# Kernel tuning notes

Hardware: AMD Instinct MI355X
Metric: run time of the kernel (lower is better)

## Reference

```python
import jax, jax.numpy as jnp
import numpy as np

B, T, I, H, D = 4, 4096, 1024, 16, 64


def setup_inputs() -> dict:
    key = jax.random.key(0)
    k1, k2, k3 = jax.random.split(key, 3)
    inputs = jax.random.normal(k1, (B, T, I), dtype=jnp.float32)
    kv_kernel = jax.random.normal(k2, (I, H, D, 2), dtype=jnp.float32) * (1.0 / np.sqrt(I))
    q_kernel = jax.random.normal(k3, (H, D), dtype=jnp.float32) * (1.0 / np.sqrt(D))
    return {"inputs": inputs, "kv_kernel": kv_kernel, "q_kernel": q_kernel}


def _combine(a, b):
    # state layout along last axis: [m (1), u (1), w (D)]
    ma, ua, wa = a[..., :1], a[..., 1:2], a[..., 2:]
    mb, ub, wb = b[..., :1], b[..., 1:2], b[..., 2:]
    m = jnp.maximum(ma, mb)
    ea = jnp.exp(ma - m)
    eb = jnp.exp(mb - m)
    return jnp.concatenate([m, ua * ea + ub * eb, wa * ea + wb * eb], axis=-1)


def reference(inputs, kv_kernel, q_kernel):
    # inputs: (B,T,I); kv_kernel: (I,H,D,2); q_kernel: (H,D)
    kv = jnp.einsum('bti,ihdk->bthdk', inputs, kv_kernel)
    kv = jax.nn.silu(kv)
    k = kv[..., 0]  # (B,T,H,D)
    v = kv[..., 1]  # (B,T,H,D)
    st = jnp.einsum('hd,bthd->bth', q_kernel, k)[..., None]  # (B,T,H,1)
    u_init = jnp.ones_like(st)
    elems = jnp.concatenate([st, u_init, v], axis=-1)  # (B,T,H,2+D)
    o = jax.lax.associative_scan(_combine, elems, axis=1)
    c = o[..., 1:2]  # denominator (B,T,H,1)
    a = o[..., 2:]   # numerator   (B,T,H,D)
    h = a / c        # (B,T,H,D)
    # concat_heads=False -> mean over heads
    return jnp.mean(h, axis=-2)  # (B,T,D)
```

## Files before the change

kernel.cpp:

```cpp
#include <hip/hip_runtime.h>
#include <hip/hip_bf16.h>
#include <math.h>

constexpr int B_ = 4, T_ = 4096, I_ = 1024, H_ = 16, D_ = 64;
constexpr int M_ = B_ * T_;
constexpr int N_ = H_ * D_ * 2;
constexpr int C_ = 64;
constexpr int L_ = T_ / C_;
constexpr int NT_ = 16;

typedef __bf16 bf16x8 __attribute__((ext_vector_type(8)));
typedef float  f32x4  __attribute__((ext_vector_type(4)));

__device__ __forceinline__ float silu_f(float x) {
    return x / (1.0f + __expf(-x));
}

__device__ __forceinline__ ushort f2bf_u(float x) {
    unsigned u = __float_as_uint(x);
    unsigned r = (u + 0x7fffu + ((u >> 16) & 1u)) >> 16;
    return (ushort)r;
}
__device__ __forceinline__ float bfu2f(ushort u) {
    return __uint_as_float(((unsigned)u) << 16);
}

__device__ __forceinline__ void gload_lds16(const void* g, void* l) {
    __builtin_amdgcn_global_load_lds(
        (const __attribute__((address_space(1))) unsigned int*)g,
        (__attribute__((address_space(3))) unsigned int*)l, 16, 0, 0);
}

__global__ __launch_bounds__(256) void convert_a_kernel(
    const float* __restrict__ A, ushort* __restrict__ A2)
{
    int idx = blockIdx.x * 256 + threadIdx.x;
    int m  = idx >> 8;
    int kq = (idx & 255) * 4;
    float4 a = *reinterpret_cast<const float4*>(&A[(size_t)m * 1024 + kq]);
    ushort4 hi;
    hi.x = f2bf_u(a.x);
    hi.y = f2bf_u(a.y);
    hi.z = f2bf_u(a.z);
    hi.w = f2bf_u(a.w);
    *reinterpret_cast<ushort4*>(&A2[(size_t)m * 1024 + kq]) = hi;
}

__global__ __launch_bounds__(256) void convert_bT_kernel(
    const float* __restrict__ Bm, ushort* __restrict__ B2T)
{
    __shared__ float tile[64][65];
    const int k0 = blockIdx.x * 64;
    const int n0 = blockIdx.y * 64;
    const int tid = threadIdx.x;
    #pragma unroll
    for (int p = 0; p < 4; ++p) {
        int f = tid + p * 256;
        int r  = f >> 4;
        int c4 = (f & 15) * 4;
        float4 v = *reinterpret_cast<const float4*>(
            &Bm[(size_t)(k0 + r) * 2048 + n0 + c4]);
        tile[r][c4 + 0] = v.x; tile[r][c4 + 1] = v.y;
        tile[r][c4 + 2] = v.z; tile[r][c4 + 3] = v.w;
    }
    __syncthreads();
    #pragma unroll
    for (int p = 0; p < 4; ++p) {
        int f = tid + p * 256;
        int n  = f >> 4;
        int kq = (f & 15) * 4;
        ushort4 hi;
        hi.x = f2bf_u(tile[kq + 0][n]);
        hi.y = f2bf_u(tile[kq + 1][n]);
        hi.z = f2bf_u(tile[kq + 2][n]);
        hi.w = f2bf_u(tile[kq + 3][n]);
        *reinterpret_cast<ushort4*>(&B2T[(size_t)(n0 + n) * 1024 + k0 + kq]) = hi;
    }
}

__device__ __forceinline__ int akof(int t) { return t * 64; }
__device__ __forceinline__ int bkof(int t) { return t * 64; }

#define BARRIER do { asm volatile("" ::: "memory"); \
    __builtin_amdgcn_s_barrier(); \
    asm volatile("" ::: "memory"); } while (0)
#define WAITLGKM asm volatile("s_waitcnt lgkmcnt(0)" ::: "memory")
#define WAITVM(n) asm volatile("s_waitcnt vmcnt(" #n ")" ::: "memory")

#define STAGE(gptr, kb, ldsoff, rs2) do { \
    gload_lds16((gptr) + (kb),         lds + (ldsoff) + tid * 8); \
    gload_lds16((gptr) + (kb) + (rs2), lds + (ldsoff) + 4096 + tid * 8); \
} while (0)

#define RDA(ab, i, kk) (*reinterpret_cast<const bf16x8*>((ab) + (i) * 1024 + ((kk) ? ck1 : ck0)))
#define RDB(bb, j, kk) (*reinterpret_cast<const bf16x8*>((bb) + (j) * 1024 + ((kk) ? ck1 : ck0)))

#define PH_READ_A(ab, ibase) do { \
    _Pragma("unroll") for (int i_ = 0; i_ < 4; ++i_) { \
        a[i_][0] = RDA(ab, (ibase) + i_, 0); \
        a[i_][1] = RDA(ab, (ibase) + i_, 1); } } while (0)
#define PH_READ_B(bb, breg, jbase) do { \
    _Pragma("unroll") for (int j_ = 0; j_ < 2; ++j_) { \
        breg[j_][0] = RDB(bb, (jbase) + j_, 0); \
        breg[j_][1] = RDB(bb, (jbase) + j_, 1); } } while (0)

#define QUAD(IH, BREG, JB) do { \
    __builtin_amdgcn_s_setprio(1); \
    _Pragma("unroll") for (int i_ = 0; i_ < 4; ++i_) \
    _Pragma("unroll") for (int j_ = 0; j_ < 2; ++j_) \
    _Pragma("unroll") for (int k_ = 0; k_ < 2; ++k_) \
        acc[(IH) + i_][(JB) + j_] = __builtin_amdgcn_mfma_f32_16x16x32_bf16( \
            a[i_][k_], BREG[j_][k_], acc[(IH) + i_][(JB) + j_], 0, 0, 0); \
    __builtin_amdgcn_s_setprio(0); \
} while (0)

__global__ __launch_bounds__(512, 2) void gemm_mfma8_kernel(
    const ushort* __restrict__ A2,
    const ushort* __restrict__ B2T,
    const float* __restrict__ qk,
    ushort* __restrict__ v_buf,
    float* __restrict__ s_buf)
{
    __shared__ ushort lds[65536];
    __shared__ float spart[8][128];

    const int bid = blockIdx.x;
    const int swz = (bid & 7) * 64 + (bid >> 3);
    const int bx  = swz >> 6;
    const int by  = swz & 63;
    const int m0  = by * 256;
    const int n0  = bx * 256;

    const int tid  = threadIdx.x;
    const int lane = tid & 63;
    const int wid  = tid >> 6;
    const int wr = wid >> 2, wc = wid & 3;
    const int l15 = lane & 15, lg = lane >> 4;

    const int row0 = tid >> 3;
    const int ch0  = (tid & 7) ^ (row0 & 7);
    const ushort* pA  = A2  + (size_t)(m0 + row0) * 1024 + ch0 * 8;
    const ushort* pB  = B2T + (size_t)(n0 + row0) * 1024 + ch0 * 8;
    const ushort* pA1 = pA + 128 * 1024;
    const ushort* pB1 = pB + 128 * 1024;

    const int ck0 = ((0 + lg) ^ (l15 & 7)) * 8;
    const int ck1 = ((4 + lg) ^ (l15 & 7)) * 8;
    const ushort* aB0 = lds + (wr * 128 + l15) * 64;
    const ushort* bB0 = lds + 16384 + (wc * 64 + l15) * 64;
    const ushort* aB1 = aB0 + 32768;
    const ushort* bB1 = bB0 + 32768;

    f32x4 acc[8][4];
    #pragma unroll
    for (int i = 0; i < 8; ++i)
        #pragma unroll
        for (int j = 0; j < 4; ++j)
            acc[i][j] = (f32x4){0.f, 0.f, 0.f, 0.f};
    bf16x8 a[4][2], b01[2][2], b23[2][2];

    {
        const int ak0 = akof(0), bk0 = bkof(0);
        const int ak1 = akof(1), bk1 = bkof(1);
        STAGE(pA,  ak0, 0,             65536);
        STAGE(pA1, ak0, 8192,          65536);
        STAGE(pB,  bk0, 16384,         65536);
        STAGE(pB1, bk0, 16384 + 8192,  65536);
        STAGE(pB,  bk1, 49152,         65536);
        STAGE(pA,  ak1, 32768,         65536);
        WAITVM(4);
        BARRIER;
    }

    for (int I = 0; I < NT_ / 2 - 1; ++I) {
        const int t1g = 2 * I + 1, t2g = 2 * I + 2, t3g = 2 * I + 3;
        const int ak1 = akof(t1g), bk1 = bkof(t1g);
        const int ak2 = akof(t2g), bk2 = bkof(t2g);
        const int ak3 = akof(t3g), bk3 = bkof(t3g);
        PH_READ_A(aB0, 0); PH_READ_B(bB0, b01, 0);
        STAGE(pA1, ak1, 32768 + 8192, 65536);
        BARRIER; WAITLGKM; QUAD(0, b01, 0); BARRIER;
        PH_READ_B(bB0, b23, 2);
        STAGE(pB1, bk1, 49152 + 8192, 65536);
        BARRIER; WAITLGKM; QUAD(0, b23, 2); BARRIER;
        PH_READ_A(aB0, 4);
        STAGE(pB, bk2, 16384, 65536);
        BARRIER; WAITLGKM; QUAD(4, b01, 0); BARRIER;
        STAGE(pA, ak2, 0, 65536);
        WAITVM(4);
        BARRIER; QUAD(4, b23, 2); BARRIER;
        PH_READ_A(aB1, 0); PH_READ_B(bB1, b01, 0);
        STAGE(pA1, ak2, 8192, 65536);
        BARRIER; WAITLGKM; QUAD(0, b01, 0); BARRIER;
        PH_READ_B(bB1, b23, 2);
        STAGE(pB1, bk2, 16384 + 8192, 65536);
        BARRIER; WAITLGKM; QUAD(0, b23, 2); BARRIER;
        PH_READ_A(aB1, 4);
        STAGE(pB, bk3, 49152, 65536);
        BARRIER; WAITLGKM; QUAD(4, b01, 0); BARRIER;
        STAGE(pA, ak3, 32768, 65536);
        WAITVM(4);
        BARRIER; QUAD(4, b23, 2); BARRIER;
    }

    {
        const int t1g = NT_ - 1;
        const int ak1 = akof(t1g), bk1 = bkof(t1g);
        PH_READ_A(aB0, 0); PH_READ_B(bB0, b01, 0);
        STAGE(pA1, ak1, 32768 + 8192, 65536);
        BARRIER; WAITLGKM; QUAD(0, b01, 0); BARRIER;
        PH_READ_B(bB0, b23, 2);
        STAGE(pB1, bk1, 49152 + 8192, 65536);
        BARRIER; WAITLGKM; QUAD(0, b23, 2); BARRIER;
        PH_READ_A(aB0, 4);
        BARRIER; WAITLGKM; QUAD(4, b01, 0); BARRIER;
        WAITVM(0);
        BARRIER; QUAD(4, b23, 2); BARRIER;
        PH_READ_A(aB1, 0); PH_READ_B(bB1, b01, 0);
        BARRIER; WAITLGKM; QUAD(0, b01, 0); BARRIER;
        PH_READ_B(bB1, b23, 2);
        BARRIER; WAITLGKM; QUAD(0, b23, 2); BARRIER;
        PH_READ_A(aB1, 4);
        BARRIER; WAITLGKM; QUAD(4, b01, 0); BARRIER;
        QUAD(4, b23, 2);
    }

    const int hloc  = wc >> 1;
    const int h     = 2 * bx + hloc;
    const int dbase = (wc & 1) * 32 + (l15 >> 1);
    float qv[4];
    #pragma unroll
    for (int j = 0; j < 4; ++j) qv[j] = qk[h * 64 + dbase + j * 8];
    const bool kcol = ((l15 & 1) == 0);

    #pragma unroll
    for (int i = 0; i < 8; ++i) {
        #pragma unroll
        for (int rr = 0; rr < 4; ++rr) {
            int m = m0 + wr * 128 + i * 16 + lg * 4 + rr;
            int b = m >> 12, tt = m & 4095;
            float p = 0.f;
            #pragma unroll
            for (int j = 0; j < 4; ++j) {
                float sv = silu_f(acc[i][j][rr]);
                if (kcol) {
                    p += qv[j] * sv;
                } else {
                    v_buf[((size_t)(b * H_ + h) * T_ + tt) * D_ + dbase + j * 8] =
                        f2bf_u(sv);
                }
            }
            p += __shfl_xor(p, 2);
            p += __shfl_xor(p, 4);
            p += __shfl_xor(p, 8);
            if (l15 == 0) spart[wid][i * 16 + lg * 4 + rr] = p;
        }
    }
    __syncthreads();
    {
        int wr2 = tid >> 8, hl = (tid >> 7) & 1, row = tid & 127;
        int m = m0 + wr2 * 128 + row;
        int b = m >> 12, tt = m & 4095;
        s_buf[(size_t)(b * H_ + 2 * bx + hl) * T_ + tt] =
            spart[wr2 * 4 + hl * 2][row] + spart[wr2 * 4 + hl * 2 + 1][row];
    }
}

#define TILE_M 128
#define TILE_N 128
#define TILE_K 16
__global__ __launch_bounds__(256) void gemm_kv_kernel(
    const float* __restrict__ A, const float* __restrict__ Bm,
    const float* __restrict__ q, ushort* __restrict__ v_buf,
    float* __restrict__ s_buf)
{
    __shared__ float As[TILE_K][TILE_M + 4];
    __shared__ float Bs[TILE_K][TILE_N + 4];
    const int tid = threadIdx.x;
    const int h   = blockIdx.x;
    const int bm  = blockIdx.y;
    const int m0  = bm * TILE_M;
    const int n0  = h * TILE_N;
    const int tx = tid & 15, ty = tid >> 4;
    float acc[8][8];
    #pragma unroll
    for (int i = 0; i < 8; ++i)
        #pragma unroll
        for (int j = 0; j < 8; ++j) acc[i][j] = 0.f;
    for (int k0 = 0; k0 < I_; k0 += TILE_K) {
        #pragma unroll
        for (int p = 0; p < 2; ++p) {
            int f = tid + p * 256;
            int row = f >> 2, kq = (f & 3) * 4;
            float4 av = *reinterpret_cast<const float4*>(
                &A[(size_t)(m0 + row) * I_ + k0 + kq]);
            As[kq + 0][row] = av.x; As[kq + 1][row] = av.y;
            As[kq + 2][row] = av.z; As[kq + 3][row] = av.w;
        }
        #pragma unroll
        for (int p = 0; p < 2; ++p) {
            int f = tid + p * 256;
            int row = f >> 5, c4 = (f & 31) * 4;
            *reinterpret_cast<float4*>(&Bs[row][c4]) =
                *reinterpret_cast<const float4*>(
                    &Bm[(size_t)(k0 + row) * N_ + n0 + c4]);
        }
        __syncthreads();
        #pragma unroll
        for (int kk = 0; kk < TILE_K; ++kk) {
            float4 a0 = *reinterpret_cast<const float4*>(&As[kk][ty * 8]);
            float4 a1 = *reinterpret_cast<const float4*>(&As[kk][ty * 8 + 4]);
            float4 b0 = *reinterpret_cast<const float4*>(&Bs[kk][tx * 8]);
            float4 b1 = *reinterpret_cast<const float4*>(&Bs[kk][tx * 8 + 4]);
            float af[8] = {a0.x, a0.y, a0.z, a0.w, a1.x, a1.y, a1.z, a1.w};
            float bf[8] = {b0.x, b0.y, b0.z, b0.w, b1.x, b1.y, b1.z, b1.w};
            #pragma unroll
            for (int i = 0; i < 8; ++i)
                #pragma unroll
                for (int j = 0; j < 8; ++j)
                    acc[i][j] = fmaf(af[i], bf[j], acc[i][j]);
        }
        __syncthreads();
    }
    float4 qv = *reinterpret_cast<const float4*>(&q[h * D_ + tx * 4]);
    float qf[4] = {qv.x, qv.y, qv.z, qv.w};
    #pragma unroll
    for (int i = 0; i < 8; ++i) {
        int m = m0 + ty * 8 + i;
        int b = m >> 12, t = m & 4095;
        float partial = 0.f;
        #pragma unroll
        for (int j = 0; j < 4; ++j) {
            float kval = silu_f(acc[i][2 * j]);
            float vv = silu_f(acc[i][2 * j + 1]);
            v_buf[((size_t)(b * H_ + h) * T_ + t) * D_ + tx * 4 + j] = f2bf_u(vv);
            partial = fmaf(qf[j], kval, partial);
        }
        #pragma unroll
        for (int mask = 8; mask >= 1; mask >>= 1)
            partial += __shfl_xor(partial, mask, 16);
        if (tx == 0) s_buf[(size_t)(b * H_ + h) * T_ + t] = partial;
    }
}

__global__ __launch_bounds__(64) void chunk_agg_kernel(
    const float* __restrict__ s_buf, const ushort* __restrict__ v_buf,
    float* __restrict__ agg_m, float* __restrict__ agg_u,
    float* __restrict__ agg_w)
{
    const int x    = blockIdx.x;
    const int c    = x & (C_ - 1);
    const int bh   = x >> 6;
    const int lane = threadIdx.x;
    const float* sp  = s_buf + (size_t)bh * T_ + c * L_;
    const ushort* vp = v_buf + ((size_t)bh * T_ + c * L_) * D_ + lane;
    float m = -INFINITY, u = 0.f, w = 0.f;
    for (int t = 0; t < L_; ++t) {
        float s  = sp[t];
        float vv = bfu2f(vp[(size_t)t * D_]);
        float mn = fmaxf(m, s);
        float ea = __expf(m - mn);
        float eb = __expf(s - mn);
        u = u * ea + eb;
        w = w * ea + vv * eb;
        m = mn;
    }
    if (lane == 0) { agg_m[x] = m; agg_u[x] = u; }
    agg_w[(size_t)x * D_ + lane] = w;
}

__global__ __launch_bounds__(64) void chunk_prefix_kernel(
    float* __restrict__ agg_m, float* __restrict__ agg_u,
    float* __restrict__ agg_w)
{
    const int bh   = blockIdx.x;
    const int lane = threadIdx.x;
    float pm = -INFINITY, pu = 0.f, pw = 0.f;
    for (int c = 0; c < C_; ++c) {
        int base = bh * C_ + c;
        float am = agg_m[base];
        float au = agg_u[base];
        float aw = agg_w[(size_t)base * D_ + lane];
        if (lane == 0) { agg_m[base] = pm; agg_u[base] = pu; }
        agg_w[(size_t)base * D_ + lane] = pw;
        float mn = fmaxf(pm, am);
        float ea = __expf(pm - mn);
        float eb = __expf(am - mn);
        pu = pu * ea + au * eb;
        pw = pw * ea + aw * eb;
        pm = mn;
    }
}

__global__ __launch_bounds__(256) void scan_apply_kernel(
    const float* __restrict__ s_buf, const ushort* __restrict__ v_buf,
    const float* __restrict__ agg_m, const float* __restrict__ agg_u,
    const float* __restrict__ agg_w, float* __restrict__ out)
{
    __shared__ float part[4][8][64];
    const int bx   = blockIdx.x;
    const int b    = bx >> 6;
    const int c    = bx & (C_ - 1);
    const int w    = threadIdx.x >> 6;
    const int lane = threadIdx.x & 63;
    float m[4], u[4], ws[4];
    #pragma unroll
    for (int j = 0; j < 4; ++j) {
        int h = w * 4 + j;
        int base = (b * H_ + h) * C_ + c;
        m[j]  = agg_m[base];
        u[j]  = agg_u[base];
        ws[j] = agg_w[(size_t)base * D_ + lane];
    }
    const int t0 = c * L_;
    for (int g = 0; g < L_ / 8; ++g) {
        #pragma unroll
        for (int qq = 0; qq < 8; ++qq) {
            int t = t0 + g * 8 + qq;
            float acc = 0.f;
            #pragma unroll
            for (int j = 0; j < 4; ++j) {
                int h = w * 4 + j;
                size_t bht = (size_t)(b * H_ + h) * T_ + t;
                float s  = s_buf[bht];
                float vv = bfu2f(v_buf[bht * D_ + lane]);
                float mn = fmaxf(m[j], s);
                float ea = __expf(m[j] - mn);
                float eb = __expf(s - mn);
                u[j]  = u[j] * ea + eb;
                ws[j] = ws[j] * ea + vv * eb;
                m[j]  = mn;
                acc += ws[j] / u[j];
            }
            part[w][qq][lane] = acc;
        }
        __syncthreads();
        {
            int e  = threadIdx.x;
            int tt = e >> 6, d = e & 63;
            float sum = part[0][tt][d] + part[1][tt][d]
                      + part[2][tt][d] + part[3][tt][d];
            out[((size_t)b * T_ + (t0 + g * 8 + tt)) * D_ + d] = sum * (1.f / 16.f);
        }
        {
            int e  = threadIdx.x + 256;
            int tt = e >> 6, d = e & 63;
            float sum = part[0][tt][d] + part[1][tt][d]
                      + part[2][tt][d] + part[3][tt][d];
            out[((size_t)b * T_ + (t0 + g * 8 + tt)) * D_ + d] = sum * (1.f / 16.f);
        }
        __syncthreads();
    }
}

extern "C" void kernel_launch(void* const* d_in, const int* in_sizes, int n_in,
                              void* d_out, int out_size, void* d_ws, size_t ws_size,
                              hipStream_t stream) {
    const float* A  = (const float*)d_in[0];
    const float* Bm = (const float*)d_in[1];
    const float* q  = (const float*)d_in[2];
    float* out = (float*)d_out;

    ushort* v_buf = (ushort*)d_ws;
    float*  s_buf = (float*)(v_buf + (size_t)B_ * H_ * T_ * D_);
    float*  agg_m = s_buf + (size_t)B_ * H_ * T_;
    float*  agg_u = agg_m + B_ * H_ * C_;
    float*  agg_w = agg_u + B_ * H_ * C_;
    ushort* A2    = (ushort*)(agg_w + (size_t)B_ * H_ * C_ * D_);
    ushort* B2T   = A2 + (size_t)M_ * 1024;

    size_t need = (size_t)B_ * H_ * T_ * D_ * 2
                + ((size_t)262144 + 4096 + 4096 + 262144) * 4
                + ((size_t)M_ * 1024 + (size_t)2048 * 1024) * 2;

    if (ws_size >= need) {
        convert_a_kernel<<<M_ * 1024 / (256 * 4), 256, 0, stream>>>(A, A2);
        convert_bT_kernel<<<dim3(16, 32), 256, 0, stream>>>(Bm, B2T);
        gemm_mfma8_kernel<<<512, 512, 0, stream>>>(A2, B2T, q, v_buf, s_buf);
    } else {
        dim3 ggrid(H_, M_ / TILE_M);
        gemm_kv_kernel<<<ggrid, 256, 0, stream>>>(A, Bm, q, v_buf, s_buf);
    }
    chunk_agg_kernel<<<B_ * H_ * C_, 64, 0, stream>>>(s_buf, v_buf, agg_m, agg_u, agg_w);
    chunk_prefix_kernel<<<B_ * H_, 64, 0, stream>>>(agg_m, agg_u, agg_w);
    scan_apply_kernel<<<B_ * C_, 256, 0, stream>>>(s_buf, v_buf, agg_m, agg_u, agg_w, out);
}
```

Before: 161.5 us.

## Make GEMM blocks persistent over two M tiles, prefetching the next during epilogue

Each GEMM block now computes two consecutive 256-row M tiles instead of one, and the grid is halved to 256 blocks. The first k-tiles of the second M tile are staged into LDS while the SiLU/score epilogue of the first tile runs, hiding load latency behind the epilogue. The block-to-tile swizzle is dropped in favour of a simple bx/bj mapping, which may change L2 reuse. With 256 blocks on 256 CUs at two blocks per CU, occupancy per CU may fall.

```diff
diff --git a/kernel.cpp b/kernel.cpp
--- a/kernel.cpp
+++ b/kernel.cpp
@@ -125,10 +125,8 @@
     __shared__ float spart[8][128];
 
     const int bid = blockIdx.x;
-    const int swz = (bid & 7) * 64 + (bid >> 3);
-    const int bx  = swz >> 6;
-    const int by  = swz & 63;
-    const int m0  = by * 256;
+    const int bx  = bid & 7;
+    const int bj  = bid >> 3;
     const int n0  = bx * 256;
 
     const int tid  = threadIdx.x;
@@ -139,9 +137,7 @@
 
     const int row0 = tid >> 3;
     const int ch0  = (tid & 7) ^ (row0 & 7);
-    const ushort* pA  = A2  + (size_t)(m0 + row0) * 1024 + ch0 * 8;
     const ushort* pB  = B2T + (size_t)(n0 + row0) * 1024 + ch0 * 8;
-    const ushort* pA1 = pA + 128 * 1024;
     const ushort* pB1 = pB + 128 * 1024;
 
     const int ck0 = ((0 + lg) ^ (l15 & 7)) * 8;
@@ -151,118 +147,144 @@
     const ushort* aB1 = aB0 + 32768;
     const ushort* bB1 = bB0 + 32768;
 
-    f32x4 acc[8][4];
-    #pragma unroll
-    for (int i = 0; i < 8; ++i)
-        #pragma unroll
-        for (int j = 0; j < 4; ++j)
-            acc[i][j] = (f32x4){0.f, 0.f, 0.f, 0.f};
-    bf16x8 a[4][2], b01[2][2], b23[2][2];
-
-    {
-        const int ak0 = akof(0), bk0 = bkof(0);
-        const int ak1 = akof(1), bk1 = bkof(1);
-        STAGE(pA,  ak0, 0,             65536);
-        STAGE(pA1, ak0, 8192,          65536);
-        STAGE(pB,  bk0, 16384,         65536);
-        STAGE(pB1, bk0, 16384 + 8192,  65536);
-        STAGE(pB,  bk1, 49152,         65536);
-        STAGE(pA,  ak1, 32768,         65536);
-        WAITVM(4);
-        BARRIER;
-    }
-
-    for (int I = 0; I < NT_ / 2 - 1; ++I) {
-        const int t1g = 2 * I + 1, t2g = 2 * I + 2, t3g = 2 * I + 3;
-        const int ak1 = akof(t1g), bk1 = bkof(t1g);
-        const int ak2 = akof(t2g), bk2 = bkof(t2g);
-        const int ak3 = akof(t3g), bk3 = bkof(t3g);
-        PH_READ_A(aB0, 0); PH_READ_B(bB0, b01, 0);
-        STAGE(pA1, ak1, 32768 + 8192, 65536);
-        BARRIER; WAITLGKM; QUAD(0, b01, 0); BARRIER;
-        PH_READ_B(bB0, b23, 2);
-        STAGE(pB1, bk1, 49152 + 8192, 65536);
-        BARRIER; WAITLGKM; QUAD(0, b23, 2); BARRIER;
-        PH_READ_A(aB0, 4);
-        STAGE(pB, bk2, 16384, 65536);
-        BARRIER; WAITLGKM; QUAD(4, b01, 0); BARRIER;
-        STAGE(pA, ak2, 0, 65536);
-        WAITVM(4);
-        BARRIER; QUAD(4, b23, 2); BARRIER;
-        PH_READ_A(aB1, 0); PH_READ_B(bB1, b01, 0);
-        STAGE(pA1, ak2, 8192, 65536);
-        BARRIER; WAITLGKM; QUAD(0, b01, 0); BARRIER;
-        PH_READ_B(bB1, b23, 2);
-        STAGE(pB1, bk2, 16384 + 8192, 65536);
-        BARRIER; WAITLGKM; QUAD(0, b23, 2); BARRIER;
-        PH_READ_A(aB1, 4);
-        STAGE(pB, bk3, 49152, 65536);
-        BARRIER; WAITLGKM; QUAD(4, b01, 0); BARRIER;
-        STAGE(pA, ak3, 32768, 65536);
-        WAITVM(4);
-        BARRIER; QUAD(4, b23, 2); BARRIER;
-    }
-
-    {
-        const int t1g = NT_ - 1;
-        const int ak1 = akof(t1g), bk1 = bkof(t1g);
-        PH_READ_A(aB0, 0); PH_READ_B(bB0, b01, 0);
-        STAGE(pA1, ak1, 32768 + 8192, 65536);
-        BARRIER; WAITLGKM; QUAD(0, b01, 0); BARRIER;
-        PH_READ_B(bB0, b23, 2);
-        STAGE(pB1, bk1, 49152 + 8192, 65536);
-        BARRIER; WAITLGKM; QUAD(0, b23, 2); BARRIER;
-        PH_READ_A(aB0, 4);
-        BARRIER; WAITLGKM; QUAD(4, b01, 0); BARRIER;
-        WAITVM(0);
-        BARRIER; QUAD(4, b23, 2); BARRIER;
-        PH_READ_A(aB1, 0); PH_READ_B(bB1, b01, 0);
-        BARRIER; WAITLGKM; QUAD(0, b01, 0); BARRIER;
-        PH_READ_B(bB1, b23, 2);
-        BARRIER; WAITLGKM; QUAD(0, b23, 2); BARRIER;
-        PH_READ_A(aB1, 4);
-        BARRIER; WAITLGKM; QUAD(4, b01, 0); BARRIER;
-        QUAD(4, b23, 2);
-    }
-
-    const int hloc  = wc >> 1;
-    const int h     = 2 * bx + hloc;
+    const int h     = 2 * bx + (wc >> 1);
     const int dbase = (wc & 1) * 32 + (l15 >> 1);
     float qv[4];
     #pragma unroll
     for (int j = 0; j < 4; ++j) qv[j] = qk[h * 64 + dbase + j * 8];
     const bool kcol = ((l15 & 1) == 0);
 
-    #pragma unroll
-    for (int i = 0; i < 8; ++i) {
-        #pragma unroll
-        for (int rr = 0; rr < 4; ++rr) {
-            int m = m0 + wr * 128 + i * 16 + lg * 4 + rr;
-            int b = m >> 12, tt = m & 4095;
-            float p = 0.f;
+    bf16x8 a[4][2], b01[2][2], b23[2][2];
+
+    {
+        const int m0 = (2 * bj) * 256;
+        const ushort* pA  = A2 + (size_t)(m0 + row0) * 1024 + ch0 * 8;
+        const ushort* pA1 = pA + 128 * 1024;
+        STAGE(pA,  akof(0), 0,             65536);
+        STAGE(pA1, akof(0), 8192,          65536);
+        STAGE(pB,  bkof(0), 16384,         65536);
+        STAGE(pB1, bkof(0), 16384 + 8192,  65536);
+        STAGE(pB,  bkof(1), 49152,         65536);
+        STAGE(pA,  akof(1), 32768,         65536);
+        WAITVM(4);
+        BARRIER;
+    }
+
+    #pragma unroll 1
+    for (int tt = 0; tt < 2; ++tt) {
+        const int m0 = (2 * bj + tt) * 256;
+        const ushort* pA  = A2 + (size_t)(m0 + row0) * 1024 + ch0 * 8;
+        const ushort* pA1 = pA + 128 * 1024;
+
+        f32x4 acc[8][4];
+        #pragma unroll
+        for (int i = 0; i < 8; ++i)
             #pragma unroll
-            for (int j = 0; j < 4; ++j) {
-                float sv = silu_f(acc[i][j][rr]);
-                if (kcol) {
-                    p += qv[j] * sv;
-                } else {
-                    v_buf[((size_t)(b * H_ + h) * T_ + tt) * D_ + dbase + j * 8] =
-                        f2bf_u(sv);
+            for (int j = 0; j < 4; ++j)
+                acc[i][j] = (f32x4){0.f, 0.f, 0.f, 0.f};
+
+        #pragma unroll 1
+        for (int I = 0; I < NT_ / 2 - 1; ++I) {
+            const int t1g = 2 * I + 1, t2g = 2 * I + 2, t3g = 2 * I + 3;
+            const int ak1 = akof(t1g), bk1 = bkof(t1g);
+            const int ak2 = akof(t2g), bk2 = bkof(t2g);
+            const int ak3 = akof(t3g), bk3 = bkof(t3g);
+            PH_READ_A(aB0, 0); PH_READ_B(bB0, b01, 0);
+            STAGE(pA1, ak1, 32768 + 8192, 65536);
+            BARRIER; WAITLGKM; QUAD(0, b01, 0); BARRIER;
+            PH_READ_B(bB0, b23, 2);
+            STAGE(pB1, bk1, 49152 + 8192, 65536);
+            BARRIER; WAITLGKM; QUAD(0, b23, 2); BARRIER;
+            PH_READ_A(aB0, 4);
+            STAGE(pB, bk2, 16384, 65536);
+            BARRIER; WAITLGKM; QUAD(4, b01, 0); BARRIER;
+            STAGE(pA, ak2, 0, 65536);
+            WAITVM(4);
+            BARRIER; QUAD(4, b23, 2); BARRIER;
+            PH_READ_A(aB1, 0); PH_READ_B(bB1, b01, 0);
+            STAGE(pA1, ak2, 8192, 65536);
+            BARRIER; WAITLGKM; QUAD(0, b01, 0); BARRIER;
+            PH_READ_B(bB1, b23, 2);
+            STAGE(pB1, bk2, 16384 + 8192, 65536);
+            BARRIER; WAITLGKM; QUAD(0, b23, 2); BARRIER;
+            PH_READ_A(aB1, 4);
+            STAGE(pB, bk3, 49152, 65536);
+            BARRIER; WAITLGKM; QUAD(4, b01, 0); BARRIER;
+            STAGE(pA, ak3, 32768, 65536);
+            WAITVM(4);
+            BARRIER; QUAD(4, b23, 2); BARRIER;
+        }
+
+        {
+            const int t1g = NT_ - 1;
+            const int ak1 = akof(t1g), bk1 = bkof(t1g);
+            PH_READ_A(aB0, 0); PH_READ_B(bB0, b01, 0);
+            STAGE(pA1, ak1, 32768 + 8192, 65536);
+            BARRIER; WAITLGKM; QUAD(0, b01, 0); BARRIER;
+            PH_READ_B(bB0, b23, 2);
+            STAGE(pB1, bk1, 49152 + 8192, 65536);
+            BARRIER; WAITLGKM; QUAD(0, b23, 2); BARRIER;
+            PH_READ_A(aB0, 4);
+            BARRIER; WAITLGKM; QUAD(4, b01, 0); BARRIER;
+            WAITVM(0);
+            BARRIER; QUAD(4, b23, 2); BARRIER;
+            PH_READ_A(aB1, 0); PH_READ_B(bB1, b01, 0);
+            BARRIER; WAITLGKM; QUAD(0, b01, 0); BARRIER;
+            PH_READ_B(bB1, b23, 2);
+            BARRIER; WAITLGKM; QUAD(0, b23, 2); BARRIER;
+            PH_READ_A(aB1, 4);
+            BARRIER; WAITLGKM; QUAD(4, b01, 0); BARRIER;
+            QUAD(4, b23, 2);
+        }
+
+        BARRIER;
+
+        if (tt == 0) {
+            const int m0n = (2 * bj + 1) * 256;
+            const ushort* qA  = A2 + (size_t)(m0n + row0) * 1024 + ch0 * 8;
+            const ushort* qA1 = qA + 128 * 1024;
+            STAGE(qA,  akof(0), 0,             65536);
+            STAGE(qA1, akof(0), 8192,          65536);
+            STAGE(pB,  bkof(0), 16384,         65536);
+            STAGE(pB1, bkof(0), 16384 + 8192,  65536);
+            STAGE(pB,  bkof(1), 49152,         65536);
+            STAGE(qA,  akof(1), 32768,         65536);
+        }
+
+        #pragma unroll
+        for (int i = 0; i < 8; ++i) {
+            #pragma unroll
+            for (int rr = 0; rr < 4; ++rr) {
+                int m = m0 + wr * 128 + i * 16 + lg * 4 + rr;
+                int b = m >> 12, ttm = m & 4095;
+                float p = 0.f;
+                #pragma unroll
+                for (int j = 0; j < 4; ++j) {
+                    float sv = silu_f(acc[i][j][rr]);
+                    if (kcol) {
+                        p += qv[j] * sv;
+                    } else {
+                        v_buf[((size_t)(b * H_ + h) * T_ + ttm) * D_ + dbase + j * 8] =
+                            f2bf_u(sv);
+                    }
                 }
+                p += __shfl_xor(p, 2);
+                p += __shfl_xor(p, 4);
+                p += __shfl_xor(p, 8);
+                if (l15 == 0) spart[wid][i * 16 + lg * 4 + rr] = p;
             }
-            p += __shfl_xor(p, 2);
-            p += __shfl_xor(p, 4);
-            p += __shfl_xor(p, 8);
-            if (l15 == 0) spart[wid][i * 16 + lg * 4 + rr] = p;
-        }
-    }
-    __syncthreads();
-    {
-        int wr2 = tid >> 8, hl = (tid >> 7) & 1, row = tid & 127;
-        int m = m0 + wr2 * 128 + row;
-        int b = m >> 12, tt = m & 4095;
-        s_buf[(size_t)(b * H_ + 2 * bx + hl) * T_ + tt] =
-            spart[wr2 * 4 + hl * 2][row] + spart[wr2 * 4 + hl * 2 + 1][row];
+        }
+        __syncthreads();
+        {
+            int wr2 = tid >> 8, hl = (tid >> 7) & 1, row = tid & 127;
+            int m = m0 + wr2 * 128 + row;
+            int b = m >> 12, ttm = m & 4095;
+            s_buf[(size_t)(b * H_ + 2 * bx + hl) * T_ + ttm] =
+                spart[wr2 * 4 + hl * 2][row] + spart[wr2 * 4 + hl * 2 + 1][row];
+        }
+        if (tt == 0) {
+            BARRIER;
+        }
     }
 }
 
@@ -476,7 +498,7 @@
     if (ws_size >= need) {
         convert_a_kernel<<<M_ * 1024 / (256 * 4), 256, 0, stream>>>(A, A2);
         convert_bT_kernel<<<dim3(16, 32), 256, 0, stream>>>(Bm, B2T);
-        gemm_mfma8_kernel<<<512, 512, 0, stream>>>(A2, B2T, q, v_buf, s_buf);
+        gemm_mfma8_kernel<<<256, 512, 0, stream>>>(A2, B2T, q, v_buf, s_buf);
     } else {
         dim3 ggrid(H_, M_ / TILE_M);
         gemm_kv_kernel<<<ggrid, 256, 0, stream>>>(A, Bm, q, v_buf, s_buf);
```

Measured after the change: 165.9 us. 1.03x slower.

## Fuse chunk aggregation into GEMM epilogue and merge conversion kernels

Applied to the files above, without the earlier changes.

The A and B fp32-to-bf16 conversion kernels become one launch whose block index picks which job to do. The GEMM epilogue now also keeps its bf16 V tile and the per-row scores in LDS, then each wave runs the per-chunk online-softmax aggregation for one head and one 64-row chunk, writing agg_m, agg_u and agg_w directly. This removes the separate chunk_agg launch and its re-read of v_buf and s_buf from global memory. The cost is a serial 64-step scan added to the GEMM tail and some extra LDS traffic, plus a few minor unroll pragmas.

```diff
diff --git a/kernel.cpp b/kernel.cpp
--- a/kernel.cpp
+++ b/kernel.cpp
@@ -31,50 +31,50 @@
         (__attribute__((address_space(3))) unsigned int*)l, 16, 0, 0);
 }
 
-__global__ __launch_bounds__(256) void convert_a_kernel(
-    const float* __restrict__ A, ushort* __restrict__ A2)
-{
-    int idx = blockIdx.x * 256 + threadIdx.x;
-    int m  = idx >> 8;
-    int kq = (idx & 255) * 4;
-    float4 a = *reinterpret_cast<const float4*>(&A[(size_t)m * 1024 + kq]);
-    ushort4 hi;
-    hi.x = f2bf_u(a.x);
-    hi.y = f2bf_u(a.y);
-    hi.z = f2bf_u(a.z);
-    hi.w = f2bf_u(a.w);
-    *reinterpret_cast<ushort4*>(&A2[(size_t)m * 1024 + kq]) = hi;
-}
-
-__global__ __launch_bounds__(256) void convert_bT_kernel(
+__global__ __launch_bounds__(256) void convert_fused_kernel(
+    const float* __restrict__ A,  ushort* __restrict__ A2,
     const float* __restrict__ Bm, ushort* __restrict__ B2T)
 {
     __shared__ float tile[64][65];
-    const int k0 = blockIdx.x * 64;
-    const int n0 = blockIdx.y * 64;
     const int tid = threadIdx.x;
-    #pragma unroll
-    for (int p = 0; p < 4; ++p) {
-        int f = tid + p * 256;
-        int r  = f >> 4;
-        int c4 = (f & 15) * 4;
-        float4 v = *reinterpret_cast<const float4*>(
-            &Bm[(size_t)(k0 + r) * 2048 + n0 + c4]);
-        tile[r][c4 + 0] = v.x; tile[r][c4 + 1] = v.y;
-        tile[r][c4 + 2] = v.z; tile[r][c4 + 3] = v.w;
-    }
-    __syncthreads();
-    #pragma unroll
-    for (int p = 0; p < 4; ++p) {
-        int f = tid + p * 256;
-        int n  = f >> 4;
-        int kq = (f & 15) * 4;
+    if (blockIdx.x < 16384) {
+        int idx = blockIdx.x * 256 + tid;
+        int m  = idx >> 8;
+        int kq = (idx & 255) * 4;
+        float4 a = *reinterpret_cast<const float4*>(&A[(size_t)m * 1024 + kq]);
         ushort4 hi;
-        hi.x = f2bf_u(tile[kq + 0][n]);
-        hi.y = f2bf_u(tile[kq + 1][n]);
-        hi.z = f2bf_u(tile[kq + 2][n]);
-        hi.w = f2bf_u(tile[kq + 3][n]);
-        *reinterpret_cast<ushort4*>(&B2T[(size_t)(n0 + n) * 1024 + k0 + kq]) = hi;
+        hi.x = f2bf_u(a.x);
+        hi.y = f2bf_u(a.y);
+        hi.z = f2bf_u(a.z);
+        hi.w = f2bf_u(a.w);
+        *reinterpret_cast<ushort4*>(&A2[(size_t)m * 1024 + kq]) = hi;
+    } else {
+        int bk = blockIdx.x - 16384;
+        const int k0 = (bk & 15) * 64;
+        const int n0 = (bk >> 4) * 64;
+        #pragma unroll
+        for (int p = 0; p < 4; ++p) {
+            int f = tid + p * 256;
+            int r  = f >> 4;
+            int c4 = (f & 15) * 4;
+            float4 v = *reinterpret_cast<const float4*>(
+                &Bm[(size_t)(k0 + r) * 2048 + n0 + c4]);
+            tile[r][c4 + 0] = v.x; tile[r][c4 + 1] = v.y;
+            tile[r][c4 + 2] = v.z; tile[r][c4 + 3] = v.w;
+        }
+        __syncthreads();
+        #pragma unroll
+        for (int p = 0; p < 4; ++p) {
+            int f = tid + p * 256;
+            int n  = f >> 4;
+            int kq = (f & 15) * 4;
+            ushort4 hi;
+            hi.x = f2bf_u(tile[kq + 0][n]);
+            hi.y = f2bf_u(tile[kq + 1][n]);
+            hi.z = f2bf_u(tile[kq + 2][n]);
+            hi.w = f2bf_u(tile[kq + 3][n]);
+            *reinterpret_cast<ushort4*>(&B2T[(size_t)(n0 + n) * 1024 + k0 + kq]) = hi;
+        }
     }
 }
 
@@ -119,10 +119,14 @@
     const ushort* __restrict__ B2T,
     const float* __restrict__ qk,
     ushort* __restrict__ v_buf,
-    float* __restrict__ s_buf)
+    float* __restrict__ s_buf,
+    float* __restrict__ agg_m,
+    float* __restrict__ agg_u,
+    float* __restrict__ agg_w)
 {
     __shared__ ushort lds[65536];
     __shared__ float spart[8][128];
+    __shared__ float s_lds[2][256];
 
     const int bid = blockIdx.x;
     const int swz = (bid & 7) * 64 + (bid >> 3);
@@ -160,18 +164,17 @@
     bf16x8 a[4][2], b01[2][2], b23[2][2];
 
     {
-        const int ak0 = akof(0), bk0 = bkof(0);
-        const int ak1 = akof(1), bk1 = bkof(1);
-        STAGE(pA,  ak0, 0,             65536);
-        STAGE(pA1, ak0, 8192,          65536);
-        STAGE(pB,  bk0, 16384,         65536);
-        STAGE(pB1, bk0, 16384 + 8192,  65536);
-        STAGE(pB,  bk1, 49152,         65536);
-        STAGE(pA,  ak1, 32768,         65536);
+        STAGE(pA,  akof(0), 0,             65536);
+        STAGE(pA1, akof(0), 8192,          65536);
+        STAGE(pB,  bkof(0), 16384,         65536);
+        STAGE(pB1, bkof(0), 16384 + 8192,  65536);
+        STAGE(pB,  bkof(1), 49152,         65536);
+        STAGE(pA,  akof(1), 32768,         65536);
         WAITVM(4);
         BARRIER;
     }
 
+    #pragma unroll 1
     for (int I = 0; I < NT_ / 2 - 1; ++I) {
         const int t1g = 2 * I + 1, t2g = 2 * I + 2, t3g = 2 * I + 3;
         const int ak1 = akof(t1g), bk1 = bkof(t1g);
@@ -224,6 +227,7 @@
         BARRIER; WAITLGKM; QUAD(4, b01, 0); BARRIER;
         QUAD(4, b23, 2);
     }
+    BARRIER;
 
     const int hloc  = wc >> 1;
     const int h     = 2 * bx + hloc;
@@ -237,7 +241,8 @@
     for (int i = 0; i < 8; ++i) {
         #pragma unroll
         for (int rr = 0; rr < 4; ++rr) {
-            int m = m0 + wr * 128 + i * 16 + lg * 4 + rr;
+            int rloc = wr * 128 + i * 16 + lg * 4 + rr;
+            int m = m0 + rloc;
             int b = m >> 12, tt = m & 4095;
             float p = 0.f;
             #pragma unroll
@@ -246,8 +251,9 @@
                 if (kcol) {
                     p += qv[j] * sv;
                 } else {
-                    v_buf[((size_t)(b * H_ + h) * T_ + tt) * D_ + dbase + j * 8] =
-                        f2bf_u(sv);
+                    ushort vb = f2bf_u(sv);
+                    v_buf[((size_t)(b * H_ + h) * T_ + tt) * D_ + dbase + j * 8] = vb;
+                    lds[hloc * 16384 + rloc * 64 + dbase + j * 8] = vb;
                 }
             }
             p += __shfl_xor(p, 2);
@@ -261,8 +267,35 @@
         int wr2 = tid >> 8, hl = (tid >> 7) & 1, row = tid & 127;
         int m = m0 + wr2 * 128 + row;
         int b = m >> 12, tt = m & 4095;
-        s_buf[(size_t)(b * H_ + 2 * bx + hl) * T_ + tt] =
-            spart[wr2 * 4 + hl * 2][row] + spart[wr2 * 4 + hl * 2 + 1][row];
+        float sval = spart[wr2 * 4 + hl * 2][row] + spart[wr2 * 4 + hl * 2 + 1][row];
+        s_buf[(size_t)(b * H_ + 2 * bx + hl) * T_ + tt] = sval;
+        s_lds[hl][wr2 * 128 + row] = sval;
+    }
+    __syncthreads();
+
+    {
+        const int h_l = wid & 1;
+        const int c_l = wid >> 1;
+        const int b   = m0 >> 12;
+        const int hg  = 2 * bx + h_l;
+        const int cg  = ((m0 & 4095) >> 6) + c_l;
+        const int base = (b * H_ + hg) * C_ + cg;
+        const ushort* vl = lds + h_l * 16384 + (c_l * 64) * 64 + lane;
+        const float*  sl = &s_lds[h_l][c_l * 64];
+        float m = -INFINITY, u = 0.f, w = 0.f;
+        #pragma unroll 8
+        for (int t = 0; t < 64; ++t) {
+            float s  = sl[t];
+            float vv = bfu2f(vl[t * 64]);
+            float mn = fmaxf(m, s);
+            float ea = __expf(m - mn);
+            float eb = __expf(s - mn);
+            u = u * ea + eb;
+            w = w * ea + vv * eb;
+            m = mn;
+        }
+        if (lane == 0) { agg_m[base] = m; agg_u[base] = u; }
+        agg_w[(size_t)base * D_ + lane] = w;
     }
 }
 
@@ -376,6 +409,7 @@
     const int bh   = blockIdx.x;
     const int lane = threadIdx.x;
     float pm = -INFINITY, pu = 0.f, pw = 0.f;
+    #pragma unroll 4
     for (int c = 0; c < C_; ++c) {
         int base = bh * C_ + c;
         float am = agg_m[base];
@@ -474,14 +508,15 @@
                 + ((size_t)M_ * 1024 + (size_t)2048 * 1024) * 2;
 
     if (ws_size >= need) {
-        convert_a_kernel<<<M_ * 1024 / (256 * 4), 256, 0, stream>>>(A, A2);
-        convert_bT_kernel<<<dim3(16, 32), 256, 0, stream>>>(Bm, B2T);
-        gemm_mfma8_kernel<<<512, 512, 0, stream>>>(A2, B2T, q, v_buf, s_buf);
+        convert_fused_kernel<<<16896, 256, 0, stream>>>(A, A2, Bm, B2T);
+        gemm_mfma8_kernel<<<512, 512, 0, stream>>>(A2, B2T, q, v_buf, s_buf,
+                                                   agg_m, agg_u, agg_w);
     } else {
         dim3 ggrid(H_, M_ / TILE_M);
         gemm_kv_kernel<<<ggrid, 256, 0, stream>>>(A, Bm, q, v_buf, s_buf);
-    }
-    chunk_agg_kernel<<<B_ * H_ * C_, 64, 0, stream>>>(s_buf, v_buf, agg_m, agg_u, agg_w);
+        chunk_agg_kernel<<<B_ * H_ * C_, 64, 0, stream>>>(s_buf, v_buf,
+                                                          agg_m, agg_u, agg_w);
+    }
     chunk_prefix_kernel<<<B_ * H_, 64, 0, stream>>>(agg_m, agg_u, agg_w);
     scan_apply_kernel<<<B_ * C_, 256, 0, stream>>>(s_buf, v_buf, agg_m, agg_u, agg_w, out);
 }
```

Result: no change. 161.0 us (-0.3%).
